# Kernel optimization log

Hardware: AMD Instinct MI355X
Metric: run time of the kernel (lower is better)

## Reference

```python
import jax, jax.numpy as jnp
import numpy as np

B, I, H = 4096, 1024, 1024
LN_EPS = 1e-5


def setup_inputs() -> dict:
    key = jax.random.key(0)
    ks = jax.random.split(key, 7)
    s = 1.0 / np.sqrt(H)  # PyTorch LSTMCell init scale
    return {
        "input": jax.random.normal(ks[0], (B, I), jnp.float32),
        "h": jax.random.normal(ks[1], (B, H), jnp.float32),
        "c": jax.random.normal(ks[2], (B, H), jnp.float32),
        "w_ih": jax.random.normal(ks[3], (4 * H, I), jnp.float32) * s,
        "w_hh": jax.random.normal(ks[4], (4 * H, H), jnp.float32) * s,
        "b_ih": jax.random.normal(ks[5], (4 * H,), jnp.float32) * s,
        "b_hh": jax.random.normal(ks[6], (4 * H,), jnp.float32) * s,
        "ln_gamma": jnp.ones((4 * H,), jnp.float32),
        "ln_beta": jnp.zeros((4 * H,), jnp.float32),
    }


def reference(input, h, c, w_ih, w_hh, b_ih, b_hh, ln_gamma, ln_beta):
    # gates: [B, 4H] = x @ W_ih^T + h @ W_hh^T + biases
    gates = (jnp.einsum("bi,gi->bg", input, w_ih)
             + jnp.einsum("bh,gh->bg", h, w_hh)
             + b_ih + b_hh)
    # LayerNorm over the 4H gate axis
    mu = jnp.mean(gates, axis=-1, keepdims=True)
    var = jnp.mean(jnp.square(gates - mu), axis=-1, keepdims=True)
    gates = (gates - mu) * jax.lax.rsqrt(var + LN_EPS) * ln_gamma + ln_beta
    # PyTorch gate order: input, forget, cell(g), output
    i_g, f_g, g_g, o_g = jnp.split(gates, 4, axis=-1)
    new_c = jax.nn.sigmoid(f_g) * c + jax.nn.sigmoid(i_g) * jnp.tanh(g_g)
    new_h = jax.nn.sigmoid(o_g) * jnp.tanh(new_c)
    return (new_h, new_c)
```

## Files before the change

kernel.cpp:

```cpp
#include <hip/hip_runtime.h>
#include <hip/hip_bf16.h>
#include <stdint.h>

#define LN_EPS 1e-5f

typedef __attribute__((ext_vector_type(8))) short bf16x8;
typedef __attribute__((ext_vector_type(4))) float f32x4;
typedef __attribute__((ext_vector_type(4))) short short4v;

__device__ __forceinline__ short f2bf(float x) {
    union { __hip_bfloat16 b; short s; } u;
    u.b = __float2bfloat16(x);
    return u.s;
}
__device__ __forceinline__ float lo_bf(unsigned v) {
    union { unsigned u; float f; } c; c.u = v << 16; return c.f;
}
__device__ __forceinline__ float hi_bf(unsigned v) {
    union { unsigned u; float f; } c; c.u = v & 0xFFFF0000u; return c.f;
}
__device__ __forceinline__ float sigm(float x) { return 1.f / (1.f + __expf(-x)); }
__device__ __forceinline__ float tanh_f(float x) {
    x = fminf(15.f, fmaxf(-15.f, x));
    float e = __expf(2.f * x);
    return (e - 1.f) / (e + 1.f);
}

__global__ __launch_bounds__(256)
void pack_all_bf16(const float* __restrict__ x, const float* __restrict__ h,
                   const float* __restrict__ wih, const float* __restrict__ whh,
                   short* __restrict__ Acat, short* __restrict__ Wcat)
{
    const int total = 4 * 1024 * 1024;
    for (int q = blockIdx.x * blockDim.x + threadIdx.x; q < total;
         q += gridDim.x * blockDim.x) {
        const int  qq  = q & (2 * 1024 * 1024 - 1);
        const bool isW = q >= 2 * 1024 * 1024;
        const float* s0 = isW ? wih : x;
        const float* s1 = isW ? whh : h;
        short* dst = isW ? Wcat : Acat;
        const long n = (long)qq << 2;
        const long r = n >> 11;
        const int  k = (int)(n & 2047);
        const float* src = (k < 1024) ? (s0 + (r << 10) + k)
                                      : (s1 + (r << 10) + (k - 1024));
        float4 v = *(const float4*)src;
        short4v o;
        o.x = f2bf(v.x); o.y = f2bf(v.y); o.z = f2bf(v.z); o.w = f2bf(v.w);
        *(short4v*)(dst + n) = o;
    }
}

#define SWZ(x) ((x) ^ (((((x) >> 7) & 7)) << 4))

__device__ __forceinline__ void stage_half(const short* __restrict__ G, int rowBase,
                                           int t, char* halfRegion, int tid)
{
    #pragma unroll
    for (int j = 0; j < 2; ++j) {
        const int p   = j * 8192 + tid * 16;
        const int l   = SWZ(p);
        const int row = l >> 7;
        const int kel = (l & 127) >> 1;
        const short* src = G + (size_t)(rowBase + row) * 2048 + t * 64 + kel;
        __builtin_amdgcn_global_load_lds(
            (const __attribute__((address_space(1))) void*)src,
            (__attribute__((address_space(3))) void*)(halfRegion + j * 8192 + ((tid >> 6) << 10)),
            16, 0, 0);
    }
}

__device__ __forceinline__ bf16x8 ldsRead(const char* region, int logical)
{
    return *(const bf16x8*)(region + SWZ(logical));
}

#define BARR()      __builtin_amdgcn_s_barrier()
#define WAIT_LGKM() do { asm volatile("s_waitcnt lgkmcnt(0)" ::: "memory"); \
                         __builtin_amdgcn_sched_barrier(0); } while (0)
#define WAIT_VM6()  asm volatile("s_waitcnt vmcnt(6)" ::: "memory")
#define WAIT_VM0()  asm volatile("s_waitcnt vmcnt(0)" ::: "memory")
#define MFMA16(a, b, c) __builtin_amdgcn_mfma_f32_16x16x32_bf16((a), (b), (c), 0, 0, 0)

__global__ __launch_bounds__(512, 2)
void gemm256_8p(const short* __restrict__ A, const short* __restrict__ B,
                unsigned short* __restrict__ C)
{
    __shared__ __align__(1024) char smem[131072];
    const int tid  = threadIdx.x;
    const int lane = tid & 63;
    const int wave = tid >> 6;
    const int wr = wave >> 2;
    const int wc = wave & 3;
    const int bx = blockIdx.x & 15, by = blockIdx.x >> 4;
    const int brow = by * 256, bcol = bx * 256;
    const int NT = 32;

    const int aBase = (wr * 128 + (lane & 15)) * 128 + ((lane >> 4) << 4);
    const int bBase = (wc * 64  + (lane & 15)) * 128 + ((lane >> 4) << 4);

    f32x4 acc[8][4] = {};
    bf16x8 aF[4][2], bF[2][2][2];

    char* Areg0 = smem;             char* Breg0 = smem + 32768;
    char* Areg1 = smem + 65536;     char* Breg1 = smem + 65536 + 32768;

    stage_half(A, brow +   0, 0, Areg0 +     0, tid);
    stage_half(A, brow + 128, 0, Areg0 + 16384, tid);
    stage_half(B, bcol +   0, 0, Breg0 +     0, tid);
    stage_half(B, bcol + 128, 0, Breg0 + 16384, tid);
    stage_half(B, bcol +   0, 1, Breg1 +     0, tid);
    stage_half(B, bcol + 128, 1, Breg1 + 16384, tid);
    stage_half(A, brow +   0, 1, Areg1 +     0, tid);
    WAIT_VM6();
    BARR();

    for (int it = 0; it < 16; ++it) {
        const int t0 = it * 2;
        #pragma unroll
        for (int hb = 0; hb < 2; ++hb) {
            const int t = t0 + hb;
            const char* Ar = hb ? Areg1 : Areg0;
            const char* Br = hb ? Breg1 : Breg0;
            char* ArN = hb ? Areg0 : Areg1;
            char* AwC = hb ? Areg1 : Areg0;
            char* BwC = hb ? Breg1 : Breg0;

            #pragma unroll
            for (int m = 0; m < 4; ++m)
                #pragma unroll
                for (int ks = 0; ks < 2; ++ks)
                    aF[m][ks] = ldsRead(Ar, aBase + m * 2048 + ks * 64);
            #pragma unroll
            for (int n = 0; n < 2; ++n)
                #pragma unroll
                for (int ks = 0; ks < 2; ++ks)
                    bF[0][n][ks] = ldsRead(Br, bBase + n * 2048 + ks * 64);
            if (t + 1 < NT) stage_half(A, brow + 128, t + 1, ArN + 16384, tid);
            BARR(); WAIT_LGKM();
            __builtin_amdgcn_s_setprio(1);
            #pragma unroll
            for (int m = 0; m < 4; ++m)
                #pragma unroll
                for (int n = 0; n < 2; ++n)
                    #pragma unroll
                    for (int ks = 0; ks < 2; ++ks)
                        acc[m][n] = MFMA16(aF[m][ks], bF[0][n][ks], acc[m][n]);
            __builtin_amdgcn_s_setprio(0);
            BARR();

            #pragma unroll
            for (int n = 0; n < 2; ++n)
                #pragma unroll
                for (int ks = 0; ks < 2; ++ks)
                    bF[1][n][ks] = ldsRead(Br, bBase + (2 + n) * 2048 + ks * 64);
            BARR(); WAIT_LGKM();
            __builtin_amdgcn_s_setprio(1);
            #pragma unroll
            for (int m = 0; m < 4; ++m)
                #pragma unroll
                for (int n = 0; n < 2; ++n)
                    #pragma unroll
                    for (int ks = 0; ks < 2; ++ks)
                        acc[m][2 + n] = MFMA16(aF[m][ks], bF[1][n][ks], acc[m][2 + n]);
            __builtin_amdgcn_s_setprio(0);
            BARR();

            #pragma unroll
            for (int m = 0; m < 4; ++m)
                #pragma unroll
                for (int ks = 0; ks < 2; ++ks)
                    aF[m][ks] = ldsRead(Ar, aBase + (4 + m) * 2048 + ks * 64);
            if (t + 2 < NT) stage_half(B, bcol + 0, t + 2, BwC + 0, tid);
            BARR(); WAIT_LGKM();
            __builtin_amdgcn_s_setprio(1);
            #pragma unroll
            for (int m = 0; m < 4; ++m)
                #pragma unroll
                for (int n = 0; n < 2; ++n)
                    #pragma unroll
                    for (int ks = 0; ks < 2; ++ks)
                        acc[4 + m][2 + n] = MFMA16(aF[m][ks], bF[1][n][ks], acc[4 + m][2 + n]);
            __builtin_amdgcn_s_setprio(0);
            BARR();

            if (t + 2 < NT) {
                stage_half(B, bcol + 128, t + 2, BwC + 16384, tid);
                stage_half(A, brow +   0, t + 2, AwC +     0, tid);
                WAIT_VM6();
            } else {
                WAIT_VM0();
            }
            BARR(); WAIT_LGKM();
            __builtin_amdgcn_s_setprio(1);
            #pragma unroll
            for (int m = 0; m < 4; ++m)
                #pragma unroll
                for (int n = 0; n < 2; ++n)
                    #pragma unroll
                    for (int ks = 0; ks < 2; ++ks)
                        acc[4 + m][n] = MFMA16(aF[m][ks], bF[0][n][ks], acc[4 + m][n]);
            __builtin_amdgcn_s_setprio(0);
            BARR();
        }
    }

    const int row0 = brow + wr * 128 + ((lane >> 4) << 2);
    const int col0 = bcol + wc * 64 + (lane & 15);
    #pragma unroll
    for (int m = 0; m < 8; ++m)
        #pragma unroll
        for (int n = 0; n < 4; ++n) {
            unsigned short* Cp = C + (size_t)(row0 + m * 16) * 4096 + col0 + n * 16;
            #pragma unroll
            for (int j = 0; j < 4; ++j)
                Cp[(size_t)j * 4096] = (unsigned short)f2bf(acc[m][n][j]);
        }
}

__global__ __launch_bounds__(256)
void ln_act_kernel(const unsigned short* __restrict__ gates,
                   const float* __restrict__ b_ih, const float* __restrict__ b_hh,
                   const float* __restrict__ gamma, const float* __restrict__ beta,
                   const float* __restrict__ c,
                   float* __restrict__ out_h, float* __restrict__ out_c)
{
    __shared__ float sg[4096];
    __shared__ float rs[4], rq[4];
    const int b = blockIdx.x;
    const int t = threadIdx.x;
    const uint4*  grow = (const uint4*)(gates + ((long)b << 12));
    const float4* bi4  = (const float4*)b_ih;
    const float4* bh4  = (const float4*)b_hh;

    float sum = 0.f, sq = 0.f;
    #pragma unroll
    for (int j = 0; j < 2; ++j) {
        const int q = t + j * 256;
        uint4 u = grow[q];
        float g8[8] = { lo_bf(u.x), hi_bf(u.x), lo_bf(u.y), hi_bf(u.y),
                        lo_bf(u.z), hi_bf(u.z), lo_bf(u.w), hi_bf(u.w) };
        float4 bi0 = bi4[2 * q], bi1 = bi4[2 * q + 1];
        float4 bh0 = bh4[2 * q], bh1 = bh4[2 * q + 1];
        g8[0] += bi0.x + bh0.x;  g8[1] += bi0.y + bh0.y;
        g8[2] += bi0.z + bh0.z;  g8[3] += bi0.w + bh0.w;
        g8[4] += bi1.x + bh1.x;  g8[5] += bi1.y + bh1.y;
        g8[6] += bi1.z + bh1.z;  g8[7] += bi1.w + bh1.w;
        ((float4*)sg)[2 * q]     = { g8[0], g8[1], g8[2], g8[3] };
        ((float4*)sg)[2 * q + 1] = { g8[4], g8[5], g8[6], g8[7] };
        #pragma unroll
        for (int e = 0; e < 8; ++e) { sum += g8[e]; sq += g8[e] * g8[e]; }
    }
    #pragma unroll
    for (int off = 32; off > 0; off >>= 1) {
        sum += __shfl_down(sum, off);
        sq  += __shfl_down(sq, off);
    }
    if ((t & 63) == 0) { rs[t >> 6] = sum; rq[t >> 6] = sq; }
    __syncthreads();
    sum = rs[0] + rs[1] + rs[2] + rs[3];
    sq  = rq[0] + rq[1] + rq[2] + rq[3];
    const float mu   = sum * (1.f / 4096.f);
    const float rstd = rsqrtf(sq * (1.f / 4096.f) - mu * mu + LN_EPS);

    const float4* sg4 = (const float4*)sg;
    const float4* gm4 = (const float4*)gamma;
    const float4* bt4 = (const float4*)beta;
    float4 vi = sg4[t],        vf = sg4[256 + t];
    float4 vg = sg4[512 + t],  vo = sg4[768 + t];
    float4 gi = gm4[t], gf = gm4[256 + t], gg = gm4[512 + t], go = gm4[768 + t];
    float4 zi = bt4[t], zf = bt4[256 + t], zg = bt4[512 + t], zo = bt4[768 + t];
    float4 cc = ((const float4*)c)[((long)b << 8) + t];
    float4 nh, nc;
    {
        float i0, f0, g0, o0;
        #define DO_COMP(X)                                                    \
            i0 = (vi.X - mu) * rstd * gi.X + zi.X;                            \
            f0 = (vf.X - mu) * rstd * gf.X + zf.X;                            \
            g0 = (vg.X - mu) * rstd * gg.X + zg.X;                            \
            o0 = (vo.X - mu) * rstd * go.X + zo.X;                            \
            nc.X = sigm(f0) * cc.X + sigm(i0) * tanh_f(g0);                   \
            nh.X = sigm(o0) * tanh_f(nc.X);
        DO_COMP(x) DO_COMP(y) DO_COMP(z) DO_COMP(w)
        #undef DO_COMP
    }
    ((float4*)out_h)[((long)b << 8) + t] = nh;
    ((float4*)out_c)[((long)b << 8) + t] = nc;
}

extern "C" void kernel_launch(void* const* d_in, const int* in_sizes, int n_in,
                              void* d_out, int out_size, void* d_ws, size_t ws_size,
                              hipStream_t stream)
{
    const float* x    = (const float*)d_in[0];
    const float* h    = (const float*)d_in[1];
    const float* c    = (const float*)d_in[2];
    const float* w_ih = (const float*)d_in[3];
    const float* w_hh = (const float*)d_in[4];
    const float* b_ih = (const float*)d_in[5];
    const float* b_hh = (const float*)d_in[6];
    const float* gam  = (const float*)d_in[7];
    const float* bet  = (const float*)d_in[8];
    float* out = (float*)d_out;
    (void)in_sizes; (void)n_in; (void)out_size; (void)ws_size;

    const int B = 4096, H = 1024;

    char*  ws    = (char*)d_ws;
    short* Acat  = (short*)ws;
    short* Wcat  = (short*)(ws + (size_t)16 * 1024 * 1024);
    unsigned short* gates = (unsigned short*)(ws + (size_t)32 * 1024 * 1024);

    pack_all_bf16<<<2048, 256, 0, stream>>>(x, h, w_ih, w_hh, Acat, Wcat);

    gemm256_8p<<<dim3(256), dim3(512), 0, stream>>>(Acat, Wcat, gates);

    ln_act_kernel<<<B, 256, 0, stream>>>(gates, b_ih, b_hh, gam, bet, c,
                                         out, out + (size_t)B * H);
}
```

Measured before the change: 214.8 us.

## Switch GEMM from 16x16x32 to 32x32x16 bf16 MFMA tiles

Replaces the 16x16x32 MFMA instruction with the 32x32x16 bf16 variant, so each wave covers its 128x64 sub-tile with 4x2 tiles of 32x32 instead of 8x4 tiles of 16x16. LDS fragment addressing, the per-phase fragment buffers and the epilogue store mapping are rewritten for the 32-lane row layout. The larger MFMA reads fewer operand fragments per flop and needs fewer instructions, easing LDS read pressure. The cost is a changed register and VGPR layout, possible new LDS bank patterns under the existing swizzle, and a less coalesced strided epilogue store.

```diff
diff --git a/kernel.cpp b/kernel.cpp
--- a/kernel.cpp
+++ b/kernel.cpp
@@ -5,7 +5,7 @@
 #define LN_EPS 1e-5f
 
 typedef __attribute__((ext_vector_type(8))) short bf16x8;
-typedef __attribute__((ext_vector_type(4))) float f32x4;
+typedef __attribute__((ext_vector_type(16))) float f32x16;
 typedef __attribute__((ext_vector_type(4))) short short4v;
 
 __device__ __forceinline__ short f2bf(float x) {
@@ -80,7 +80,7 @@
                          __builtin_amdgcn_sched_barrier(0); } while (0)
 #define WAIT_VM6()  asm volatile("s_waitcnt vmcnt(6)" ::: "memory")
 #define WAIT_VM0()  asm volatile("s_waitcnt vmcnt(0)" ::: "memory")
-#define MFMA16(a, b, c) __builtin_amdgcn_mfma_f32_16x16x32_bf16((a), (b), (c), 0, 0, 0)
+#define MFMA32(a, b, c) __builtin_amdgcn_mfma_f32_32x32x16_bf16((a), (b), (c), 0, 0, 0)
 
 __global__ __launch_bounds__(512, 2)
 void gemm256_8p(const short* __restrict__ A, const short* __restrict__ B,
@@ -96,11 +96,14 @@
     const int brow = by * 256, bcol = bx * 256;
     const int NT = 32;
 
-    const int aBase = (wr * 128 + (lane & 15)) * 128 + ((lane >> 4) << 4);
-    const int bBase = (wc * 64  + (lane & 15)) * 128 + ((lane >> 4) << 4);
-
-    f32x4 acc[8][4] = {};
-    bf16x8 aF[4][2], bF[2][2][2];
+    const int aBase = (wr * 128 + (lane & 31)) * 128 + ((lane >> 5) << 4);
+    const int bBase = (wc * 64  + (lane & 31)) * 128 + ((lane >> 5) << 4);
+
+    f32x16 acc[4][2] = {};
+    bf16x8 aF[2][2];
+    bf16x8 aH[2][4];
+    bf16x8 b01[2][2];
+    bf16x8 b23[2][2];
 
     char* Areg0 = smem;             char* Breg0 = smem + 32768;
     char* Areg1 = smem + 65536;     char* Breg1 = smem + 65536 + 32768;
@@ -127,60 +130,65 @@
             char* BwC = hb ? Breg1 : Breg0;
 
             #pragma unroll
-            for (int m = 0; m < 4; ++m)
-                #pragma unroll
-                for (int ks = 0; ks < 2; ++ks)
-                    aF[m][ks] = ldsRead(Ar, aBase + m * 2048 + ks * 64);
+            for (int m = 0; m < 2; ++m)
+                #pragma unroll
+                for (int k = 0; k < 2; ++k)
+                    aF[m][k] = ldsRead(Ar, aBase + m * 4096 + k * 32);
             #pragma unroll
             for (int n = 0; n < 2; ++n)
                 #pragma unroll
-                for (int ks = 0; ks < 2; ++ks)
-                    bF[0][n][ks] = ldsRead(Br, bBase + n * 2048 + ks * 64);
+                for (int k = 0; k < 2; ++k)
+                    b01[n][k] = ldsRead(Br, bBase + n * 4096 + k * 32);
             if (t + 1 < NT) stage_half(A, brow + 128, t + 1, ArN + 16384, tid);
             BARR(); WAIT_LGKM();
             __builtin_amdgcn_s_setprio(1);
             #pragma unroll
-            for (int m = 0; m < 4; ++m)
-                #pragma unroll
-                for (int n = 0; n < 2; ++n)
+            for (int k = 0; k < 2; ++k)
+                #pragma unroll
+                for (int m = 0; m < 2; ++m)
                     #pragma unroll
-                    for (int ks = 0; ks < 2; ++ks)
-                        acc[m][n] = MFMA16(aF[m][ks], bF[0][n][ks], acc[m][n]);
+                    for (int n = 0; n < 2; ++n)
+                        acc[m][n] = MFMA32(aF[m][k], b01[n][k], acc[m][n]);
             __builtin_amdgcn_s_setprio(0);
             BARR();
 
             #pragma unroll
+            for (int m = 0; m < 2; ++m)
+                #pragma unroll
+                for (int k = 0; k < 2; ++k)
+                    aF[m][k] = ldsRead(Ar, aBase + m * 4096 + (2 + k) * 32);
+            #pragma unroll
             for (int n = 0; n < 2; ++n)
                 #pragma unroll
-                for (int ks = 0; ks < 2; ++ks)
-                    bF[1][n][ks] = ldsRead(Br, bBase + (2 + n) * 2048 + ks * 64);
+                for (int k = 0; k < 2; ++k)
+                    b23[n][k] = ldsRead(Br, bBase + n * 4096 + (2 + k) * 32);
             BARR(); WAIT_LGKM();
             __builtin_amdgcn_s_setprio(1);
             #pragma unroll
-            for (int m = 0; m < 4; ++m)
-                #pragma unroll
-                for (int n = 0; n < 2; ++n)
+            for (int k = 0; k < 2; ++k)
+                #pragma unroll
+                for (int m = 0; m < 2; ++m)
                     #pragma unroll
-                    for (int ks = 0; ks < 2; ++ks)
-                        acc[m][2 + n] = MFMA16(aF[m][ks], bF[1][n][ks], acc[m][2 + n]);
+                    for (int n = 0; n < 2; ++n)
+                        acc[m][n] = MFMA32(aF[m][k], b23[n][k], acc[m][n]);
             __builtin_amdgcn_s_setprio(0);
             BARR();
 
             #pragma unroll
-            for (int m = 0; m < 4; ++m)
-                #pragma unroll
-                for (int ks = 0; ks < 2; ++ks)
-                    aF[m][ks] = ldsRead(Ar, aBase + (4 + m) * 2048 + ks * 64);
+            for (int m = 0; m < 2; ++m)
+                #pragma unroll
+                for (int k = 0; k < 4; ++k)
+                    aH[m][k] = ldsRead(Ar, aBase + (2 + m) * 4096 + k * 32);
             if (t + 2 < NT) stage_half(B, bcol + 0, t + 2, BwC + 0, tid);
             BARR(); WAIT_LGKM();
             __builtin_amdgcn_s_setprio(1);
             #pragma unroll
-            for (int m = 0; m < 4; ++m)
-                #pragma unroll
-                for (int n = 0; n < 2; ++n)
+            for (int k = 0; k < 2; ++k)
+                #pragma unroll
+                for (int m = 0; m < 2; ++m)
                     #pragma unroll
-                    for (int ks = 0; ks < 2; ++ks)
-                        acc[4 + m][2 + n] = MFMA16(aF[m][ks], bF[1][n][ks], acc[4 + m][2 + n]);
+                    for (int n = 0; n < 2; ++n)
+                        acc[2 + m][n] = MFMA32(aH[m][k], b01[n][k], acc[2 + m][n]);
             __builtin_amdgcn_s_setprio(0);
             BARR();
 
@@ -194,27 +202,28 @@
             BARR(); WAIT_LGKM();
             __builtin_amdgcn_s_setprio(1);
             #pragma unroll
-            for (int m = 0; m < 4; ++m)
-                #pragma unroll
-                for (int n = 0; n < 2; ++n)
+            for (int k = 0; k < 2; ++k)
+                #pragma unroll
+                for (int m = 0; m < 2; ++m)
                     #pragma unroll
-                    for (int ks = 0; ks < 2; ++ks)
-                        acc[4 + m][n] = MFMA16(aF[m][ks], bF[0][n][ks], acc[4 + m][n]);
+                    for (int n = 0; n < 2; ++n)
+                        acc[2 + m][n] = MFMA32(aH[m][2 + k], b23[n][k], acc[2 + m][n]);
             __builtin_amdgcn_s_setprio(0);
             BARR();
         }
     }
 
-    const int row0 = brow + wr * 128 + ((lane >> 4) << 2);
-    const int col0 = bcol + wc * 64 + (lane & 15);
     #pragma unroll
-    for (int m = 0; m < 8; ++m)
+    for (int m = 0; m < 4; ++m)
         #pragma unroll
-        for (int n = 0; n < 4; ++n) {
-            unsigned short* Cp = C + (size_t)(row0 + m * 16) * 4096 + col0 + n * 16;
-            #pragma unroll
-            for (int j = 0; j < 4; ++j)
-                Cp[(size_t)j * 4096] = (unsigned short)f2bf(acc[m][n][j]);
+        for (int n = 0; n < 2; ++n) {
+            const int colg  = bcol + wc * 64 + n * 32 + (lane & 31);
+            const int rbase = brow + wr * 128 + m * 32 + ((lane >> 5) << 2);
+            #pragma unroll
+            for (int r = 0; r < 16; ++r) {
+                const int row = rbase + (r & 3) + 8 * (r >> 2);
+                C[(size_t)row * 4096 + colg] = (unsigned short)f2bf(acc[m][n][r]);
+            }
         }
 }
 
```

New measurement: 218.8 us. Within noise of the previous version (+1.9%).

## Prefetch LDS fragments one phase ahead and use partial lgkmcnt waits

Applied to the files above, without the earlier changes.

Restructures the GEMM main loop so that A/B fragments for the next phase, including the next k-tile's first fragments, are read from LDS during the previous MFMA phase. Full lgkmcnt(0) waits are replaced with partial counts, so MFMAs can start while later LDS reads are still in flight. It also reorders the MFMA loops with ks outermost. The cost is extra fragment registers, which at 512 threads with launch bounds (512,2) could spill or lower occupancy, and the partial wait counts are fragile because global_load_lds may also touch the lgkm counter.

```diff
diff --git a/kernel.cpp b/kernel.cpp
--- a/kernel.cpp
+++ b/kernel.cpp
@@ -76,7 +76,7 @@
 }
 
 #define BARR()      __builtin_amdgcn_s_barrier()
-#define WAIT_LGKM() do { asm volatile("s_waitcnt lgkmcnt(0)" ::: "memory"); \
+#define LGKMN(n)    do { asm volatile("s_waitcnt lgkmcnt(" #n ")" ::: "memory"); \
                          __builtin_amdgcn_sched_barrier(0); } while (0)
 #define WAIT_VM6()  asm volatile("s_waitcnt vmcnt(6)" ::: "memory")
 #define WAIT_VM0()  asm volatile("s_waitcnt vmcnt(0)" ::: "memory")
@@ -100,7 +100,10 @@
     const int bBase = (wc * 64  + (lane & 15)) * 128 + ((lane >> 4) << 4);
 
     f32x4 acc[8][4] = {};
-    bf16x8 aF[4][2], bF[2][2][2];
+    bf16x8 fa[4][2];
+    bf16x8 fah[4][2];
+    bf16x8 fb23[2][2];
+    bf16x8 fb01[2][2][2];
 
     char* Areg0 = smem;             char* Breg0 = smem + 32768;
     char* Areg1 = smem + 65536;     char* Breg1 = smem + 65536 + 32768;
@@ -115,72 +118,75 @@
     WAIT_VM6();
     BARR();
 
+    #pragma unroll
+    for (int m = 0; m < 4; ++m)
+        #pragma unroll
+        for (int ks = 0; ks < 2; ++ks)
+            fa[m][ks] = ldsRead(Areg0, aBase + m * 2048 + ks * 64);
+    #pragma unroll
+    for (int n = 0; n < 2; ++n)
+        #pragma unroll
+        for (int ks = 0; ks < 2; ++ks)
+            fb01[0][n][ks] = ldsRead(Breg0, bBase + n * 2048 + ks * 64);
+
     for (int it = 0; it < 16; ++it) {
         const int t0 = it * 2;
         #pragma unroll
         for (int hb = 0; hb < 2; ++hb) {
             const int t = t0 + hb;
-            const char* Ar = hb ? Areg1 : Areg0;
-            const char* Br = hb ? Breg1 : Breg0;
-            char* ArN = hb ? Areg0 : Areg1;
+            const char* Ar  = hb ? Areg1 : Areg0;
+            const char* Br  = hb ? Breg1 : Breg0;
+            const char* ArN = hb ? Areg0 : Areg1;
+            const char* BrN = hb ? Breg0 : Breg1;
+            char* AwN = hb ? Areg0 : Areg1;
             char* AwC = hb ? Areg1 : Areg0;
             char* BwC = hb ? Breg1 : Breg0;
 
             #pragma unroll
+            for (int n = 0; n < 2; ++n)
+                #pragma unroll
+                for (int ks = 0; ks < 2; ++ks)
+                    fb23[n][ks] = ldsRead(Br, bBase + (2 + n) * 2048 + ks * 64);
+            if (t + 1 < NT) stage_half(A, brow + 128, t + 1, AwN + 16384, tid);
+            BARR(); LGKMN(4);
+            __builtin_amdgcn_s_setprio(1);
+            #pragma unroll
+            for (int ks = 0; ks < 2; ++ks)
+                #pragma unroll
+                for (int m = 0; m < 4; ++m)
+                    #pragma unroll
+                    for (int n = 0; n < 2; ++n)
+                        acc[m][n] = MFMA16(fa[m][ks], fb01[hb][n][ks], acc[m][n]);
+            __builtin_amdgcn_s_setprio(0);
+            BARR();
+
+            #pragma unroll
             for (int m = 0; m < 4; ++m)
                 #pragma unroll
                 for (int ks = 0; ks < 2; ++ks)
-                    aF[m][ks] = ldsRead(Ar, aBase + m * 2048 + ks * 64);
-            #pragma unroll
-            for (int n = 0; n < 2; ++n)
-                #pragma unroll
-                for (int ks = 0; ks < 2; ++ks)
-                    bF[0][n][ks] = ldsRead(Br, bBase + n * 2048 + ks * 64);
-            if (t + 1 < NT) stage_half(A, brow + 128, t + 1, ArN + 16384, tid);
-            BARR(); WAIT_LGKM();
+                    fah[m][ks] = ldsRead(Ar, aBase + (4 + m) * 2048 + ks * 64);
+            BARR(); LGKMN(8);
             __builtin_amdgcn_s_setprio(1);
             #pragma unroll
-            for (int m = 0; m < 4; ++m)
-                #pragma unroll
-                for (int n = 0; n < 2; ++n)
-                    #pragma unroll
-                    for (int ks = 0; ks < 2; ++ks)
-                        acc[m][n] = MFMA16(aF[m][ks], bF[0][n][ks], acc[m][n]);
+            for (int ks = 0; ks < 2; ++ks)
+                #pragma unroll
+                for (int m = 0; m < 4; ++m)
+                    #pragma unroll
+                    for (int n = 0; n < 2; ++n)
+                        acc[m][2 + n] = MFMA16(fa[m][ks], fb23[n][ks], acc[m][2 + n]);
             __builtin_amdgcn_s_setprio(0);
             BARR();
 
-            #pragma unroll
-            for (int n = 0; n < 2; ++n)
-                #pragma unroll
-                for (int ks = 0; ks < 2; ++ks)
-                    bF[1][n][ks] = ldsRead(Br, bBase + (2 + n) * 2048 + ks * 64);
-            BARR(); WAIT_LGKM();
+            if (t + 2 < NT) stage_half(B, bcol + 0, t + 2, BwC + 0, tid);
+            BARR(); LGKMN(0);
             __builtin_amdgcn_s_setprio(1);
             #pragma unroll
-            for (int m = 0; m < 4; ++m)
-                #pragma unroll
-                for (int n = 0; n < 2; ++n)
-                    #pragma unroll
-                    for (int ks = 0; ks < 2; ++ks)
-                        acc[m][2 + n] = MFMA16(aF[m][ks], bF[1][n][ks], acc[m][2 + n]);
-            __builtin_amdgcn_s_setprio(0);
-            BARR();
-
-            #pragma unroll
-            for (int m = 0; m < 4; ++m)
-                #pragma unroll
-                for (int ks = 0; ks < 2; ++ks)
-                    aF[m][ks] = ldsRead(Ar, aBase + (4 + m) * 2048 + ks * 64);
-            if (t + 2 < NT) stage_half(B, bcol + 0, t + 2, BwC + 0, tid);
-            BARR(); WAIT_LGKM();
-            __builtin_amdgcn_s_setprio(1);
-            #pragma unroll
-            for (int m = 0; m < 4; ++m)
-                #pragma unroll
-                for (int n = 0; n < 2; ++n)
-                    #pragma unroll
-                    for (int ks = 0; ks < 2; ++ks)
-                        acc[4 + m][2 + n] = MFMA16(aF[m][ks], bF[1][n][ks], acc[4 + m][2 + n]);
+            for (int ks = 0; ks < 2; ++ks)
+                #pragma unroll
+                for (int m = 0; m < 4; ++m)
+                    #pragma unroll
+                    for (int n = 0; n < 2; ++n)
+                        acc[4 + m][2 + n] = MFMA16(fah[m][ks], fb23[n][ks], acc[4 + m][2 + n]);
             __builtin_amdgcn_s_setprio(0);
             BARR();
 
@@ -191,15 +197,28 @@
             } else {
                 WAIT_VM0();
             }
-            BARR(); WAIT_LGKM();
+            if (t + 1 < NT) {
+                #pragma unroll
+                for (int m = 0; m < 4; ++m)
+                    #pragma unroll
+                    for (int ks = 0; ks < 2; ++ks)
+                        fa[m][ks] = ldsRead(ArN, aBase + m * 2048 + ks * 64);
+                #pragma unroll
+                for (int n = 0; n < 2; ++n)
+                    #pragma unroll
+                    for (int ks = 0; ks < 2; ++ks)
+                        fb01[hb ^ 1][n][ks] = ldsRead(BrN, bBase + n * 2048 + ks * 64);
+            }
+            BARR();
+            if (t + 1 < NT) { LGKMN(12); } else { LGKMN(0); }
             __builtin_amdgcn_s_setprio(1);
             #pragma unroll
-            for (int m = 0; m < 4; ++m)
-                #pragma unroll
-                for (int n = 0; n < 2; ++n)
-                    #pragma unroll
-                    for (int ks = 0; ks < 2; ++ks)
-                        acc[4 + m][n] = MFMA16(aF[m][ks], bF[0][n][ks], acc[4 + m][n]);
+            for (int ks = 0; ks < 2; ++ks)
+                #pragma unroll
+                for (int m = 0; m < 4; ++m)
+                    #pragma unroll
+                    for (int n = 0; n < 2; ++n)
+                        acc[4 + m][n] = MFMA16(fah[m][ks], fb01[hb][n][ks], acc[4 + m][n]);
             __builtin_amdgcn_s_setprio(0);
             BARR();
         }
```

Measured after the change: 354.0 us. +64.8%, slower.
